# Kernel optimization log

Hardware: AMD Instinct MI355X
Metric: run time of the kernel (lower is better)

The kernel has to match this reference:

```python
import jax, jax.numpy as jnp
import numpy as np

N_BINS = 15


def setup_inputs() -> dict:
    key = jax.random.key(0)
    k1, k2 = jax.random.split(key)
    N, C = 1_000_000, 100
    logits = jax.random.normal(k1, (N, C), dtype=jnp.float32)
    labels = jax.random.randint(k2, (N,), 0, C)
    return {"logits": logits, "labels": labels}


def reference(logits, labels):
    # softmax -> per-sample confidence (max prob) and prediction (argmax)
    probs = jax.nn.softmax(logits, axis=1)
    confidences = jnp.max(probs, axis=1)                      # [N]
    predictions = jnp.argmax(probs, axis=1)                   # [N]
    accuracies = (predictions == labels).astype(jnp.float32)  # [N]

    # Bin assignment equivalent to conf in (lower, upper] with equal bins on (0,1].
    # softmax max-prob is always > 0, so ceil(conf*B)-1 lands in the torch bin.
    bin_id = jnp.clip(
        jnp.ceil(confidences * N_BINS).astype(jnp.int32) - 1, 0, N_BINS - 1
    )

    ones = jnp.ones_like(confidences)
    counts = jax.ops.segment_sum(ones, bin_id, num_segments=N_BINS)        # [B]
    conf_sum = jax.ops.segment_sum(confidences, bin_id, num_segments=N_BINS)
    acc_sum = jax.ops.segment_sum(accuracies, bin_id, num_segments=N_BINS)

    n = confidences.shape[0]
    safe_counts = jnp.maximum(counts, 1.0)
    gap = jnp.abs(conf_sum / safe_counts - acc_sum / safe_counts)          # [B]
    # weighted by proportion of samples in bin; empty bins contribute 0
    ece = jnp.sum(jnp.where(counts > 0, gap * (counts / n), 0.0))
    return ece.reshape(1)
```

## Files before the change

### kernel.cpp

```cpp
#include <hip/hip_runtime.h>
#include <math.h>

#define N_BINS 15
#define LOG2E 1.44269504088896340736f

template <int CTRL>
__device__ __forceinline__ float dpp_xor(float x) {
    int xi = __builtin_bit_cast(int, x);
    int r  = __builtin_amdgcn_update_dpp(xi, xi, CTRL, 0xF, 0xF, false);
    return __builtin_bit_cast(float, r);
}

__global__ __launch_bounds__(256) void ece_main(const float* __restrict__ logits,
                                                const int* __restrict__ labels,
                                                float* __restrict__ ws,
                                                int N, int C) {
    __shared__ float s_bins[3][N_BINS];
    const int tid = threadIdx.x;
    if (tid < 3 * N_BINS) (&s_bins[0][0])[tid] = 0.f;
    __syncthreads();

    const int sl = tid & 15;
    const int group   = (blockIdx.x * blockDim.x + tid) >> 4;
    const int ngroups = (gridDim.x * blockDim.x) >> 4;

    if (C == 100) {
        const bool h = (sl < 9);
        for (int row = group; row < N; row += ngroups) {
            const float4* rp4 = (const float4*)(logits + (size_t)row * 100);
            float4 a = rp4[sl];
            float4 b;
            if (h) b = rp4[16 + sl];
            else   b = make_float4(-INFINITY, -INFINITY, -INFINITY, -INFINITY);

            float m = fmaxf(fmaxf(fmaxf(a.x, a.y), fmaxf(a.z, a.w)),
                            fmaxf(fmaxf(b.x, b.y), fmaxf(b.z, b.w)));
            m = fmaxf(m, dpp_xor<0xB1>(m));
            m = fmaxf(m, dpp_xor<0x1B>(m));
            m = fmaxf(m, dpp_xor<0x141>(m));
            m = fmaxf(m, dpp_xor<0x140>(m));

            float t = -m * LOG2E;
            float s = exp2f(fmaf(a.x, LOG2E, t)) + exp2f(fmaf(a.y, LOG2E, t))
                    + exp2f(fmaf(a.z, LOG2E, t)) + exp2f(fmaf(a.w, LOG2E, t))
                    + exp2f(fmaf(b.x, LOG2E, t)) + exp2f(fmaf(b.y, LOG2E, t))
                    + exp2f(fmaf(b.z, LOG2E, t)) + exp2f(fmaf(b.w, LOG2E, t));
            s += dpp_xor<0xB1>(s);
            s += dpp_xor<0x1B>(s);
            s += dpp_xor<0x141>(s);
            s += dpp_xor<0x140>(s);

            if (sl == 0) {
                float conf = 1.0f / s;
                int bin = (int)ceilf(conf * (float)N_BINS) - 1;
                bin = min(max(bin, 0), N_BINS - 1);
                int lab = labels[row];
                float vl = logits[(size_t)row * 100 + lab];
                atomicAdd(&s_bins[0][bin], 1.0f);
                atomicAdd(&s_bins[1][bin], conf);
                atomicAdd(&s_bins[2][bin], (vl == m) ? 1.0f : 0.0f);
            }
        }
    } else {
        for (int row = group; row < N; row += ngroups) {
            const float* rp = logits + (size_t)row * C;
            float m = -INFINITY; int mi = C;
            for (int j = sl; j < C; j += 16) {
                float v = rp[j];
                if (v > m) { m = v; mi = j; }
            }
            #pragma unroll
            for (int off = 1; off < 16; off <<= 1) {
                float om = __shfl_xor(m, off);
                int   oi = __shfl_xor(mi, off);
                if (om > m || (om == m && oi < mi)) { m = om; mi = oi; }
            }
            float s = 0.f;
            for (int j = sl; j < C; j += 16) s += __expf(rp[j] - m);
            #pragma unroll
            for (int off = 1; off < 16; off <<= 1) s += __shfl_xor(s, off);
            if (sl == 0) {
                float conf = 1.0f / s;
                int bin = (int)ceilf(conf * (float)N_BINS) - 1;
                bin = min(max(bin, 0), N_BINS - 1);
                float acc = (mi == labels[row]) ? 1.0f : 0.0f;
                atomicAdd(&s_bins[0][bin], 1.0f);
                atomicAdd(&s_bins[1][bin], conf);
                atomicAdd(&s_bins[2][bin], acc);
            }
        }
    }

    __syncthreads();
    if (tid < N_BINS) {
        atomicAdd(&ws[tid],              s_bins[0][tid]);
        atomicAdd(&ws[N_BINS + tid],     s_bins[1][tid]);
        atomicAdd(&ws[2 * N_BINS + tid], s_bins[2][tid]);
    }
}

__global__ void ece_final(const float* __restrict__ ws, float* __restrict__ out, float invN) {
    if (threadIdx.x == 0 && blockIdx.x == 0) {
        float ece = 0.f;
        for (int b = 0; b < N_BINS; ++b) {
            float c = ws[b];
            if (c > 0.f) {
                float conf_m = ws[N_BINS + b] / c;
                float acc_m  = ws[2 * N_BINS + b] / c;
                ece += fabsf(conf_m - acc_m) * (c * invN);
            }
        }
        out[0] = ece;
    }
}

extern "C" void kernel_launch(void* const* d_in, const int* in_sizes, int n_in,
                              void* d_out, int out_size, void* d_ws, size_t ws_size,
                              hipStream_t stream) {
    const float* logits = (const float*)d_in[0];
    const int*   labels = (const int*)d_in[1];
    const int N = in_sizes[1];
    const int C = in_sizes[0] / N;
    float* ws = (float*)d_ws;

    hipMemsetAsync(ws, 0, 3 * N_BINS * sizeof(float), stream);

    const int threads = 256;
    const int blocks = 2048;
    ece_main<<<blocks, threads, 0, stream>>>(logits, labels, ws, N, C);
    ece_final<<<1, 64, 0, stream>>>(ws, (float*)d_out, 1.0f / (float)N);
}
```

Baseline: 568.7 us.

## Batch four rows per group and replace dependent label-logit gather with ballot

New measurement: 549.0 us. -3.5%, faster.

```diff
diff --git a/kernel.cpp b/kernel.cpp
--- a/kernel.cpp
+++ b/kernel.cpp
@@ -11,55 +11,93 @@
     return __builtin_bit_cast(float, r);
 }
 
-__global__ __launch_bounds__(256) void ece_main(const float* __restrict__ logits,
-                                                const int* __restrict__ labels,
-                                                float* __restrict__ ws,
-                                                int N, int C) {
-    __shared__ float s_bins[3][N_BINS];
+__device__ __forceinline__ float group_max(float m) {
+    m = fmaxf(m, dpp_xor<0xB1>(m));
+    m = fmaxf(m, dpp_xor<0x1B>(m));
+    m = fmaxf(m, dpp_xor<0x141>(m));
+    m = fmaxf(m, dpp_xor<0x140>(m));
+    return m;
+}
+__device__ __forceinline__ float group_sum(float s) {
+    s += dpp_xor<0xB1>(s);
+    s += dpp_xor<0x1B>(s);
+    s += dpp_xor<0x141>(s);
+    s += dpp_xor<0x140>(s);
+    return s;
+}
+
+__device__ __forceinline__ void row_body(float4 a, float4 b, int lab, int sl,
+                                         int group16, float* s_bins ) {
+    float m = fmaxf(fmaxf(fmaxf(a.x, a.y), fmaxf(a.z, a.w)),
+                    fmaxf(fmaxf(b.x, b.y), fmaxf(b.z, b.w)));
+    m = group_max(m);
+
+    float t = -m * LOG2E;
+    float s = exp2f(fmaf(a.x, LOG2E, t)) + exp2f(fmaf(a.y, LOG2E, t))
+            + exp2f(fmaf(a.z, LOG2E, t)) + exp2f(fmaf(a.w, LOG2E, t))
+            + exp2f(fmaf(b.x, LOG2E, t)) + exp2f(fmaf(b.y, LOG2E, t))
+            + exp2f(fmaf(b.z, LOG2E, t)) + exp2f(fmaf(b.w, LOG2E, t));
+    s = group_sum(s);
+
+    int q = lab >> 2, c = lab & 3;
+    float pick = -INFINITY;
+    if (q == sl)           pick = (c == 0 ? a.x : c == 1 ? a.y : c == 2 ? a.z : a.w);
+    else if (q - 16 == sl) pick = (c == 0 ? b.x : c == 1 ? b.y : c == 2 ? b.z : b.w);
+    unsigned long long mask = __ballot(pick == m);
+
+    if (sl == 0) {
+        float conf = 1.0f / s;
+        int bin = (int)ceilf(conf * (float)N_BINS) - 1;
+        bin = min(max(bin, 0), N_BINS - 1);
+        float acc = ((mask >> (group16 * 16)) & 0xFFFFull) ? 1.0f : 0.0f;
+        atomicAdd(&s_bins[bin], 1.0f);
+        atomicAdd(&s_bins[N_BINS + bin], conf);
+        atomicAdd(&s_bins[2 * N_BINS + bin], acc);
+    }
+}
+
+__global__ __launch_bounds__(256, 4) void ece_main(const float* __restrict__ logits,
+                                                   const int* __restrict__ labels,
+                                                   float* __restrict__ ws,
+                                                   int N, int C) {
+    __shared__ float s_bins[3 * N_BINS];
     const int tid = threadIdx.x;
-    if (tid < 3 * N_BINS) (&s_bins[0][0])[tid] = 0.f;
+    if (tid < 3 * N_BINS) s_bins[tid] = 0.f;
     __syncthreads();
 
     const int sl = tid & 15;
+    const int group16 = (tid >> 4) & 3;
     const int group   = (blockIdx.x * blockDim.x + tid) >> 4;
     const int ngroups = (gridDim.x * blockDim.x) >> 4;
 
     if (C == 100) {
         const bool h = (sl < 9);
-        for (int row = group; row < N; row += ngroups) {
-            const float4* rp4 = (const float4*)(logits + (size_t)row * 100);
-            float4 a = rp4[sl];
-            float4 b;
-            if (h) b = rp4[16 + sl];
-            else   b = make_float4(-INFINITY, -INFINITY, -INFINITY, -INFINITY);
+        int row = group;
+        for (; row + 3 * ngroups < N; row += 4 * ngroups) {
+            const int r0 = row, r1 = row + ngroups, r2 = row + 2 * ngroups, r3 = row + 3 * ngroups;
+            const float4* p0 = (const float4*)(logits + (size_t)r0 * 100);
+            const float4* p1 = (const float4*)(logits + (size_t)r1 * 100);
+            const float4* p2 = (const float4*)(logits + (size_t)r2 * 100);
+            const float4* p3 = (const float4*)(logits + (size_t)r3 * 100);
+            float4 a0 = p0[sl], a1 = p1[sl], a2 = p2[sl], a3 = p3[sl];
+            float4 b0, b1, b2, b3;
+            if (h) { b0 = p0[16 + sl]; b1 = p1[16 + sl]; b2 = p2[16 + sl]; b3 = p3[16 + sl]; }
+            else {
+                b0 = b1 = b2 = b3 = make_float4(-INFINITY, -INFINITY, -INFINITY, -INFINITY);
+            }
+            int l0 = labels[r0], l1 = labels[r1], l2 = labels[r2], l3 = labels[r3];
 
-            float m = fmaxf(fmaxf(fmaxf(a.x, a.y), fmaxf(a.z, a.w)),
-                            fmaxf(fmaxf(b.x, b.y), fmaxf(b.z, b.w)));
-            m = fmaxf(m, dpp_xor<0xB1>(m));
-            m = fmaxf(m, dpp_xor<0x1B>(m));
-            m = fmaxf(m, dpp_xor<0x141>(m));
-            m = fmaxf(m, dpp_xor<0x140>(m));
-
-            float t = -m * LOG2E;
-            float s = exp2f(fmaf(a.x, LOG2E, t)) + exp2f(fmaf(a.y, LOG2E, t))
-                    + exp2f(fmaf(a.z, LOG2E, t)) + exp2f(fmaf(a.w, LOG2E, t))
-                    + exp2f(fmaf(b.x, LOG2E, t)) + exp2f(fmaf(b.y, LOG2E, t))
-                    + exp2f(fmaf(b.z, LOG2E, t)) + exp2f(fmaf(b.w, LOG2E, t));
-            s += dpp_xor<0xB1>(s);
-            s += dpp_xor<0x1B>(s);
-            s += dpp_xor<0x141>(s);
-            s += dpp_xor<0x140>(s);
-
-            if (sl == 0) {
-                float conf = 1.0f / s;
-                int bin = (int)ceilf(conf * (float)N_BINS) - 1;
-                bin = min(max(bin, 0), N_BINS - 1);
-                int lab = labels[row];
-                float vl = logits[(size_t)row * 100 + lab];
-                atomicAdd(&s_bins[0][bin], 1.0f);
-                atomicAdd(&s_bins[1][bin], conf);
-                atomicAdd(&s_bins[2][bin], (vl == m) ? 1.0f : 0.0f);
-            }
+            row_body(a0, b0, l0, sl, group16, s_bins);
+            row_body(a1, b1, l1, sl, group16, s_bins);
+            row_body(a2, b2, l2, sl, group16, s_bins);
+            row_body(a3, b3, l3, sl, group16, s_bins);
+        }
+        for (; row < N; row += ngroups) {
+            const float4* p = (const float4*)(logits + (size_t)row * 100);
+            float4 a = p[sl];
+            float4 b = h ? p[16 + sl] : make_float4(-INFINITY, -INFINITY, -INFINITY, -INFINITY);
+            int lab = labels[row];
+            row_body(a, b, lab, sl, group16, s_bins);
         }
     } else {
         for (int row = group; row < N; row += ngroups) {
@@ -84,18 +122,18 @@
                 int bin = (int)ceilf(conf * (float)N_BINS) - 1;
                 bin = min(max(bin, 0), N_BINS - 1);
                 float acc = (mi == labels[row]) ? 1.0f : 0.0f;
-                atomicAdd(&s_bins[0][bin], 1.0f);
-                atomicAdd(&s_bins[1][bin], conf);
-                atomicAdd(&s_bins[2][bin], acc);
+                atomicAdd(&s_bins[bin], 1.0f);
+                atomicAdd(&s_bins[N_BINS + bin], conf);
+                atomicAdd(&s_bins[2 * N_BINS + bin], acc);
             }
         }
     }
 
     __syncthreads();
     if (tid < N_BINS) {
-        atomicAdd(&ws[tid],              s_bins[0][tid]);
-        atomicAdd(&ws[N_BINS + tid],     s_bins[1][tid]);
-        atomicAdd(&ws[2 * N_BINS + tid], s_bins[2][tid]);
+        atomicAdd(&ws[tid],              s_bins[tid]);
+        atomicAdd(&ws[N_BINS + tid],     s_bins[N_BINS + tid]);
+        atomicAdd(&ws[2 * N_BINS + tid], s_bins[2 * N_BINS + tid]);
     }
 }
 
```
